# Optimization experiments

Hardware: AMD Instinct MI355X
Metric: run time of the kernel (lower is better)

Reference implementation:

```python
import jax, jax.numpy as jnp
import numpy as np
import math
from jax import lax

EPS = 1e-5  # BatchNorm1d default eps
K = 7       # causal conv kernel size
H = 5       # number of heads in block 2


def _cconv(x, w, b):
    # CausalConv1d: left-pad by (K-1)*dilation = 6, then valid conv. x: [B,C,L], w: [O,I,K]
    y = lax.conv_general_dilated(x, w, window_strides=(1,), padding=[(K - 1, 0)],
                                 dimension_numbers=('NCH', 'OIH', 'NCH'))
    return y + b[None, :, None]


def _bn(x, g, b):
    # BatchNorm1d in training mode: batch stats over (N, L) per channel, biased variance
    m = x.mean((0, 2), keepdims=True)
    v = ((x - m) ** 2).mean((0, 2), keepdims=True)
    return g[None, :, None] * (x - m) * lax.rsqrt(v + EPS) + b[None, :, None]


def _attn(x1, x2, x3, scale):
    # sigmoid(((X1 @ X2^T) / sqrt(L)) @ X3); x*: [B,C,L]
    s = jnp.einsum('bcl,bdl->bcd', x1, x2) * scale
    return jax.nn.sigmoid(jnp.einsum('bcd,bdl->bcl', s, x3))


def _attn_heads(x1, x2, x3, scale):
    # 5 heads chunked along L (contiguous chunks) -> vectorized over head axis
    B, C, L = x1.shape
    r = lambda x: x.reshape(B, C, H, L // H)
    x1r, x2r, x3r = r(x1), r(x2), r(x3)
    s = jnp.einsum('bchk,bdhk->bhcd', x1r, x2r) * scale  # scale uses full L, as in source
    a = jax.nn.sigmoid(jnp.einsum('bhcd,bdhk->bchk', s, x3r))
    return a.reshape(B, C, L)


def setup_inputs() -> dict:
    key = jax.random.key(0)
    ks = jax.random.split(key, 20)
    B, C, L = 64, 30, 200
    CL = C * L
    cs = (C * K) ** -0.5   # conv weight scale
    ls = CL ** -0.5        # linear weight scale
    d = {}
    d['X'] = jax.random.normal(ks[0], (B, C, L), jnp.float32)
    for i, nm in enumerate(['b1c1', 'b1c2', 'b1c3', 'b2c1', 'b2c2', 'b2c3']):
        d[nm + '_w'] = jax.random.normal(ks[1 + i], (C, C, K), jnp.float32) * cs
        d[nm + '_b'] = jax.random.normal(ks[7 + i], (C,), jnp.float32) * cs
    for nm in ['bn11', 'bn12', 'bn21', 'bn22']:
        d[nm + '_g'] = jnp.ones((C,), jnp.float32)
        d[nm + '_b'] = jnp.zeros((C,), jnp.float32)
    d['lin1_w'] = jax.random.normal(ks[13], (CL, CL), jnp.float32) * ls
    d['lin1_b'] = jax.random.normal(ks[14], (CL,), jnp.float32) * ls
    d['lin2_w'] = jax.random.normal(ks[15], (CL, CL), jnp.float32) * ls
    d['lin2_b'] = jax.random.normal(ks[16], (CL,), jnp.float32) * ls
    d['cw'] = jax.random.normal(ks[17], (CL, 2 * CL), jnp.float32) * (2 * CL) ** -0.5
    d['cb'] = jax.random.normal(ks[18], (CL,), jnp.float32) * (2 * CL) ** -0.5
    return d


def reference(X, b1c1_w, b1c1_b, b1c2_w, b1c2_b, b1c3_w, b1c3_b,
              bn11_g, bn11_b, lin1_w, lin1_b, lin2_w, lin2_b, bn12_g, bn12_b,
              b2c1_w, b2c1_b, b2c2_w, b2c2_b, b2c3_w, b2c3_b,
              bn21_g, bn21_b, bn22_g, bn22_b, cw, cb):
    B, C, L = X.shape
    scale = 1.0 / math.sqrt(L)
    # block 1: single-head sigmoid attention
    a1 = _attn(_cconv(X, b1c1_w, b1c1_b), _cconv(X, b1c2_w, b1c2_b),
               _cconv(X, b1c3_w, b1c3_b), scale)
    a1 = _bn(a1 + X, bn11_g, bn11_b)
    a1f = a1.reshape(B, -1)
    o1 = (a1f @ lin1_w.T + lin1_b) @ lin2_w.T + lin2_b  # dropout is eval-mode identity
    out1 = _bn(a1 + o1.reshape(B, C, L), bn12_g, bn12_b)
    # block 2: 5-head sigmoid attention
    a2 = _attn_heads(_cconv(X, b2c1_w, b2c1_b), _cconv(X, b2c2_w, b2c2_b),
                     _cconv(X, b2c3_w, b2c3_b), scale)
    a2 = _bn(a2 + X, bn21_g, bn21_b)
    a2f = a2.reshape(B, -1)
    # NOTE: source reuses b1_linearchain for block 2 (b2_linearchain is unused)
    o2 = (a2f @ lin1_w.T + lin1_b) @ lin2_w.T + lin2_b
    out2 = _bn(a2 + o2.reshape(B, C, L), bn22_g, bn22_b)
    # converge
    out = jnp.concatenate([out1, out2], axis=1).reshape(B, -1)  # [B, 2*C*L]
    out = out @ cw.T + cb                                       # [B, C*L]
    return out.reshape(B, 30, -1)
```

## Files before the change

### kernel.cpp

```cpp
#include <hip/hip_runtime.h>
#include <hip/hip_bf16.h>
#include <math.h>

typedef __attribute__((ext_vector_type(4))) float f32x4;
typedef __attribute__((ext_vector_type(8))) __bf16 bf16x8;
typedef __attribute__((ext_vector_type(8))) unsigned short u16x8;

__device__ __forceinline__ unsigned short f2bfu(float f) {
    unsigned u = __builtin_bit_cast(unsigned, f);
    u += 0x7fffu + ((u >> 16) & 1u);
    return (unsigned short)(u >> 16);
}

__device__ __forceinline__ bf16x8 to_bf8(f32x4 x, f32x4 y) {
    bf16x8 o;
#pragma unroll
    for (int j = 0; j < 4; ++j) { o[j] = (__bf16)x[j]; o[j + 4] = (__bf16)y[j]; }
    return o;
}

__device__ __forceinline__ void gload_lds16(const void* g, void* l) {
    __builtin_amdgcn_global_load_lds(
        (__attribute__((address_space(1))) const void*)g,
        (__attribute__((address_space(3))) void*)l, 16, 0, 0);
}

template <int VMPS>
__device__ __forceinline__ void wait_newer(int newer) {
    if (newer >= 2) {
        if constexpr (VMPS == 6) asm volatile("s_waitcnt vmcnt(12)" ::: "memory");
        else                     asm volatile("s_waitcnt vmcnt(10)" ::: "memory");
    } else if (newer == 1) {
        if constexpr (VMPS == 6) asm volatile("s_waitcnt vmcnt(6)" ::: "memory");
        else                     asm volatile("s_waitcnt vmcnt(5)" ::: "memory");
    } else {
        asm volatile("s_waitcnt vmcnt(0)" ::: "memory");
    }
}

struct ConvArgs {
    const float* w[6];
    const float* b[6];
};

__global__ __launch_bounds__(256) void conv_all(const float* __restrict__ X,
                                                ConvArgs args,
                                                float* __restrict__ out) {
    __shared__ float Xsp[30][208];
    __shared__ float Wg[30][212];
    const int b = blockIdx.x, j = blockIdx.y;
    const int tid = threadIdx.x;
    const float* xb = X + (size_t)b * 6000;
    for (int i = tid; i < 30 * 208; i += 256) {
        const int ci = i / 208, p = i - ci * 208;
        float v = 0.f;
        if (p >= 6 && p < 206) v = xb[ci * 200 + (p - 6)];
        Xsp[ci][p] = v;
    }
    const float* wsrc = args.w[j];
    for (int i = tid; i < 6300; i += 256) Wg[i / 210][i % 210] = wsrc[i];
    __syncthreads();
    if (tid < 240) {
        const int c = tid >> 3;
        const int strip = tid & 7;
        const int l0 = strip * 25;
        float acc[25];
        const float bias = args.b[j][c];
#pragma unroll
        for (int o = 0; o < 25; ++o) acc[o] = bias;
        for (int ci = 0; ci < 30; ++ci) {
            float wv[7];
#pragma unroll
            for (int kk = 0; kk < 7; ++kk) wv[kk] = Wg[c][ci * 7 + kk];
            float xw[31];
#pragma unroll
            for (int i = 0; i < 31; ++i) xw[i] = Xsp[ci][l0 + i];
#pragma unroll
            for (int o = 0; o < 25; ++o) {
                float a = acc[o];
#pragma unroll
                for (int kk = 0; kk < 7; ++kk) a += xw[o + kk] * wv[kk];
                acc[o] = a;
            }
        }
        float* op = out + ((size_t)j * 64 + b) * 6000 + c * 200 + l0;
#pragma unroll
        for (int o = 0; o < 25; ++o) op[o] = acc[o];
    }
}

__global__ __launch_bounds__(256) void attn_k(const float* __restrict__ conv,
                                              const float* __restrict__ X,
                                              float* __restrict__ A_lin) {
    __shared__ float x1s[30][204], x2s[30][204], x3s[30][204];
    __shared__ float S[5][30][30];
    const int b = blockIdx.x, blk = blockIdx.y;
    const int tid = threadIdx.x;
    const f32x4* c1 = (const f32x4*)(conv + (((size_t)blk * 3 + 0) * 64 + b) * 6000);
    const f32x4* c2 = (const f32x4*)(conv + (((size_t)blk * 3 + 1) * 64 + b) * 6000);
    const f32x4* c3 = (const f32x4*)(conv + (((size_t)blk * 3 + 2) * 64 + b) * 6000);
    for (int i = tid; i < 1500; i += 256) {
        const int c = i / 50, q = i - c * 50;
        *(f32x4*)&x1s[c][q * 4] = c1[i];
        *(f32x4*)&x2s[c][q * 4] = c2[i];
        *(f32x4*)&x3s[c][q * 4] = c3[i];
    }
    __syncthreads();
    const float scale = 7.0710678118654752e-2f;
    if (blk == 0) {
        for (int idx = tid; idx < 900; idx += 256) {
            const int c = idx / 30, d = idx - c * 30;
            f32x4 a4 = {};
            for (int q = 0; q < 50; ++q) {
                const f32x4 x = *(const f32x4*)&x1s[c][q * 4];
                const f32x4 y = *(const f32x4*)&x2s[d][q * 4];
                a4 += x * y;
            }
            S[0][c][d] = (a4[0] + a4[1] + a4[2] + a4[3]) * scale;
        }
    } else {
        for (int idx = tid; idx < 4500; idx += 256) {
            const int h = idx / 900, rem = idx - h * 900;
            const int c = rem / 30, d = rem - c * 30;
            f32x4 a4 = {};
            for (int q = 0; q < 10; ++q) {
                const f32x4 x = *(const f32x4*)&x1s[c][h * 40 + q * 4];
                const f32x4 y = *(const f32x4*)&x2s[d][h * 40 + q * 4];
                a4 += x * y;
            }
            S[h][c][d] = (a4[0] + a4[1] + a4[2] + a4[3]) * scale;
        }
    }
    __syncthreads();
    const float* Xb = X + (size_t)b * 6000;
    float* Ab = A_lin + ((size_t)blk * 64 + b) * 6000;
    for (int u = tid; u < 1500; u += 256) {
        const int c = u / 50, q = u - c * 50;
        const int hh = (blk == 0) ? 0 : (q / 10);
        f32x4 a4 = {};
        for (int d = 0; d < 30; ++d) {
            const float sv = S[hh][c][d];
            const f32x4 v = *(const f32x4*)&x3s[d][q * 4];
            a4 += sv * v;
        }
        const f32x4 xv = *(const f32x4*)(Xb + c * 200 + q * 4);
        f32x4 o;
#pragma unroll
        for (int jj = 0; jj < 4; ++jj)
            o[jj] = 1.f / (1.f + __expf(-a4[jj])) + xv[jj];
        *(f32x4*)(Ab + c * 200 + q * 4) = o;
    }
}

__global__ __launch_bounds__(256) void bn_fused1(float* __restrict__ A,
                                                 unsigned short* __restrict__ Ab,
                                                 const float* __restrict__ g11,
                                                 const float* __restrict__ b11,
                                                 const float* __restrict__ g21,
                                                 const float* __restrict__ b21) {
    const int c = blockIdx.x, h = blockIdx.y, bs = blockIdx.z;
    const int tid = threadIdx.x;
    const size_t cbase = (size_t)h * 64 * 6000 + c * 200;
    float s = 0.f, ss = 0.f;
    for (int i = tid; i < 12800; i += 256) {
        const int b = i / 200, l = i - b * 200;
        const float v = A[cbase + (size_t)b * 6000 + l];
        s += v; ss += v * v;
    }
    for (int off = 32; off > 0; off >>= 1) { s += __shfl_down(s, off); ss += __shfl_down(ss, off); }
    __shared__ float rs[4], rss[4];
    __shared__ float sc_sh, sh_sh;
    const int wave = tid >> 6, lane = tid & 63;
    if (lane == 0) { rs[wave] = s; rss[wave] = ss; }
    __syncthreads();
    if (tid == 0) {
        const float S = rs[0] + rs[1] + rs[2] + rs[3];
        const float SS = rss[0] + rss[1] + rss[2] + rss[3];
        const float mean = S * (1.f / 12800.f);
        const float var = SS * (1.f / 12800.f) - mean * mean;
        const float* gp = h ? g21 : g11;
        const float* bp = h ? b21 : b11;
        const float scale = gp[c] * rsqrtf(var + 1e-5f);
        sc_sh = scale;
        sh_sh = bp[c] - mean * scale;
    }
    __syncthreads();
    const float scale = sc_sh, shift = sh_sh;
    for (int i = tid; i < 1600; i += 256) {
        const int b = bs * 8 + i / 200, l = i % 200;
        const size_t idx = ((size_t)h * 64 + b) * 6000 + c * 200 + l;
        const float o = A[idx] * scale + shift;
        A[idx] = o;
        Ab[((size_t)h * 64 + b) * 6016 + c * 200 + l] = f2bfu(o);
    }
    if (c == 0) {
        for (int i = tid; i < 8 * 16; i += 256) {
            const int b = bs * 8 + (i >> 4);
            Ab[((size_t)h * 64 + b) * 6016 + 6000 + (i & 15)] = 0;
        }
    }
}

__global__ __launch_bounds__(256) void bn_fused2(const float* __restrict__ A,
                                                 const float* __restrict__ O,
                                                 unsigned short* __restrict__ Cat,
                                                 const float* __restrict__ g12,
                                                 const float* __restrict__ b12,
                                                 const float* __restrict__ g22,
                                                 const float* __restrict__ b22) {
    const int c = blockIdx.x, h = blockIdx.y, bs = blockIdx.z;
    const int tid = threadIdx.x;
    const size_t cbase = (size_t)h * 64 * 6000 + c * 200;
    float s = 0.f, ss = 0.f;
    for (int i = tid; i < 12800; i += 256) {
        const int b = i / 200, l = i - b * 200;
        const size_t idx = cbase + (size_t)b * 6000 + l;
        const float v = A[idx] + O[idx];
        s += v; ss += v * v;
    }
    for (int off = 32; off > 0; off >>= 1) { s += __shfl_down(s, off); ss += __shfl_down(ss, off); }
    __shared__ float rs[4], rss[4];
    __shared__ float sc_sh, sh_sh;
    const int wave = tid >> 6, lane = tid & 63;
    if (lane == 0) { rs[wave] = s; rss[wave] = ss; }
    __syncthreads();
    if (tid == 0) {
        const float S = rs[0] + rs[1] + rs[2] + rs[3];
        const float SS = rss[0] + rss[1] + rss[2] + rss[3];
        const float mean = S * (1.f / 12800.f);
        const float var = SS * (1.f / 12800.f) - mean * mean;
        const float* gp = h ? g22 : g12;
        const float* bp = h ? b22 : b12;
        const float scale = gp[c] * rsqrtf(var + 1e-5f);
        sc_sh = scale;
        sh_sh = bp[c] - mean * scale;
    }
    __syncthreads();
    const float scale = sc_sh, shift = sh_sh;
    for (int i = tid; i < 1600; i += 256) {
        const int b = bs * 8 + i / 200, l = i % 200;
        const size_t idx = ((size_t)h * 64 + b) * 6000 + c * 200 + l;
        const float o = (A[idx] + O[idx]) * scale + shift;
        Cat[(size_t)b * 12000 + (size_t)h * 6000 + c * 200 + l] = f2bfu(o);
    }
}

template <int MT>
__global__ __launch_bounds__(256) void gemm_pipe(const unsigned short* __restrict__ A,
                                                 const float* __restrict__ W,
                                                 unsigned short* __restrict__ P,
                                                 int N, int K, int KA,
                                                 int iters_total, int iters_per) {
    constexpr int M = MT * 16;
    constexpr int WB = 128 * 32 * 4;
    constexpr int AB = M * 32 * 2;
    constexpr int ACH = AB / 1024;
    constexpr int BUFSZ = WB + AB;
    constexpr int VMPS = 4 + ACH / 4;
    __shared__ __align__(16) char lds[3][BUFSZ];

    const int tid = threadIdx.x;
    const int wave = tid >> 6;
    const int lane = tid & 63;
    const int r = lane & 15;
    const int g = lane >> 4;
    const int n0 = blockIdx.x * 128;
    const int s = blockIdx.y;
    const int it0 = s * iters_per;
    int it1 = it0 + iters_per;
    if (it1 > iters_total) it1 = iters_total;
    const int nst = it1 - it0;

    f32x4 acc[MT][2] = {};

    const float* wbase[4];
    const float* wclamp[4];
    int kth[4];
#pragma unroll
    for (int u = 0; u < 4; ++u) {
        const int c = wave + 4 * u;
        const int slot = c * 64 + lane;
        const int row = slot >> 3, jj = slot & 7;
        const int j = jj ^ (row & 7);
        int rn = n0 + row;
        if (rn > N - 1) rn = N - 1;
        wbase[u] = W + (size_t)rn * K + j * 4;
        wclamp[u] = W + (size_t)rn * K + (K - 4);
        kth[u] = K - 4 - j * 4;
    }
    const unsigned short* abase[ACH / 4];
#pragma unroll
    for (int u = 0; u < ACH / 4; ++u) {
        const int c = wave + 4 * u;
        const int slot = c * 64 + lane;
        const int m = slot >> 2, jj = slot & 3;
        const int j = jj ^ ((m >> 1) & 3);
        abase[u] = A + (size_t)m * KA + j * 8;
    }

    auto stage = [&](char* base, int it) {
        const int k0 = it * 32;
#pragma unroll
        for (int u = 0; u < 4; ++u) {
            const float* src = (k0 <= kth[u]) ? (wbase[u] + k0) : wclamp[u];
            gload_lds16(src, base + (wave + 4 * u) * 1024);
        }
        char* ab = base + WB;
#pragma unroll
        for (int u = 0; u < ACH / 4; ++u) {
            gload_lds16(abase[u] + k0, ab + (wave + 4 * u) * 1024);
        }
    };

    auto compute = [&](const char* base) {
        const float* Wb = (const float*)base;
        const unsigned short* Ab = (const unsigned short*)(base + WB);
        bf16x8 bfrag[2];
#pragma unroll
        for (int nt = 0; nt < 2; ++nt) {
            const int wr = (wave + 4 * nt) * 16 + r;
            const f32x4* Wrow = (const f32x4*)(Wb + wr * 32);
            bfrag[nt] = to_bf8(Wrow[(2 * g) ^ (r & 7)], Wrow[(2 * g + 1) ^ (r & 7)]);
        }
#pragma unroll
        for (int mt = 0; mt < MT; ++mt) {
            const int m = mt * 16 + r;
            const bf16x8 afrag = __builtin_bit_cast(
                bf16x8, ((const u16x8*)(Ab + (size_t)m * 32))[g ^ ((m >> 1) & 3)]);
            acc[mt][0] = __builtin_amdgcn_mfma_f32_16x16x32_bf16(afrag, bfrag[0], acc[mt][0], 0, 0, 0);
            acc[mt][1] = __builtin_amdgcn_mfma_f32_16x16x32_bf16(afrag, bfrag[1], acc[mt][1], 0, 0, 0);
        }
    };

    if (nst > 0) {
        const int p = nst < 3 ? nst : 3;
        stage(&lds[0][0], it0);
        if (p > 1) stage(&lds[1][0], it0 + 1);
        if (p > 2) stage(&lds[2][0], it0 + 2);
        wait_newer<VMPS>(p - 1);
        __builtin_amdgcn_s_barrier();
        __builtin_amdgcn_sched_barrier(0);

        int bi = 0;
        for (int it = it0; it < it1; ++it) {
            compute(&lds[bi][0]);
            __builtin_amdgcn_sched_barrier(0);
            __builtin_amdgcn_s_barrier();
            if (it + 3 < it1) stage(&lds[bi][0], it + 3);
            if (it + 1 < it1) {
                const int last = it1 - 1;
                const int newer = ((it + 3 < last ? it + 3 : last)) - (it + 1);
                wait_newer<VMPS>(newer);
                __builtin_amdgcn_s_barrier();
                __builtin_amdgcn_sched_barrier(0);
            }
            bi = bi == 2 ? 0 : bi + 1;
        }
    }

    unsigned short* Pp = P + (size_t)s * M * N;
#pragma unroll
    for (int nt = 0; nt < 2; ++nt) {
        const int col = n0 + (wave + 4 * nt) * 16 + r;
        if (col < N) {
#pragma unroll
            for (int mt = 0; mt < MT; ++mt) {
#pragma unroll
                for (int rr = 0; rr < 4; ++rr) {
                    const int row = mt * 16 + g * 4 + rr;
                    Pp[(size_t)row * N + col] = f2bfu(acc[mt][nt][rr]);
                }
            }
        }
    }
}

template <bool OUT_BF16>
__global__ __launch_bounds__(256) void reduce_bias(const unsigned short* __restrict__ P,
                                                   const float* __restrict__ bias,
                                                   int KS, int MN, int N, int KOUT,
                                                   float* __restrict__ of,
                                                   unsigned short* __restrict__ ob) {
    const int gid0 = blockIdx.x * 256 + threadIdx.x;
    const int gstr = gridDim.x * 256;
    for (int idx = gid0; idx < MN; idx += gstr) {
        float v = bias[idx % N];
        for (int s = 0; s < KS; ++s) {
            const unsigned u = P[(size_t)s * MN + idx];
            v += __builtin_bit_cast(float, u << 16);
        }
        if constexpr (OUT_BF16) ob[(size_t)(idx / N) * KOUT + (idx % N)] = f2bfu(v);
        else of[idx] = v;
    }
    if constexpr (OUT_BF16) {
        if (KOUT > N) {
            const int M = MN / N, PADW = KOUT - N;
            for (int i = gid0; i < M * PADW; i += gstr)
                ob[(size_t)(i / PADW) * KOUT + N + (i % PADW)] = 0;
        }
    }
}

extern "C" void kernel_launch(void* const* d_in, const int* in_sizes, int n_in,
                              void* d_out, int out_size, void* d_ws, size_t ws_size,
                              hipStream_t stream) {
    (void)in_sizes; (void)n_in; (void)out_size;
    const float* X = (const float*)d_in[0];
    ConvArgs ca;
    for (int j = 0; j < 6; ++j) {
        ca.w[j] = (const float*)d_in[1 + 2 * j];
        ca.b[j] = (const float*)d_in[2 + 2 * j];
    }
    const float* bn11_g = (const float*)d_in[13];
    const float* bn11_b = (const float*)d_in[14];
    const float* bn12_g = (const float*)d_in[15];
    const float* bn12_b = (const float*)d_in[16];
    const float* bn21_g = (const float*)d_in[17];
    const float* bn21_b = (const float*)d_in[18];
    const float* bn22_g = (const float*)d_in[19];
    const float* bn22_b = (const float*)d_in[20];
    const float* lin1_w = (const float*)d_in[21];
    const float* lin1_b = (const float*)d_in[22];
    const float* lin2_w = (const float*)d_in[23];
    const float* lin2_b = (const float*)d_in[24];
    const float* cw = (const float*)d_in[25];
    const float* cb = (const float*)d_in[26];
    float* out = (float*)d_out;

    char* w = (char*)d_ws;
    float* A_lin = (float*)w;
    unsigned short* A_bf = (unsigned short*)(w + 3072000);
    char* U = w + 4612096;
    float* convout = (float*)U;
    unsigned short* T_bf = (unsigned short*)U;
    float* O = (float*)(U + 1540096);
    unsigned short* Cat = (unsigned short*)(U + 4612096);
    unsigned short* P = (unsigned short*)(w + 13832192);

    const size_t avail = ws_size > 13832192 ? ws_size - 13832192 : 0;
    int KS12 = (int)(avail / 1536000);
    if (KS12 > 10) KS12 = 10;
    if (KS12 < 1) KS12 = 1;
    int KS3 = (int)(avail / 768000);
    if (KS3 > 10) KS3 = 10;
    if (KS3 < 1) KS3 = 1;

    conv_all<<<dim3(64, 6), 256, 0, stream>>>(X, ca, convout);
    attn_k<<<dim3(64, 2), 256, 0, stream>>>(convout, X, A_lin);
    bn_fused1<<<dim3(30, 2, 8), 256, 0, stream>>>(A_lin, A_bf, bn11_g, bn11_b, bn21_g, bn21_b);

    {
        const int it_tot = 188;
        const int it_per = (it_tot + KS12 - 1) / KS12;
        gemm_pipe<8><<<dim3(47, KS12), 256, 0, stream>>>(A_bf, lin1_w, P, 6000, 6000, 6016, it_tot, it_per);
        reduce_bias<true><<<dim3(768), 256, 0, stream>>>(P, lin1_b, KS12, 768000, 6000, 6016, nullptr, T_bf);
        gemm_pipe<8><<<dim3(47, KS12), 256, 0, stream>>>(T_bf, lin2_w, P, 6000, 6000, 6016, it_tot, it_per);
        reduce_bias<false><<<dim3(768), 256, 0, stream>>>(P, lin2_b, KS12, 768000, 6000, 6000, O, nullptr);
    }

    bn_fused2<<<dim3(30, 2, 8), 256, 0, stream>>>(A_lin, O, Cat, bn12_g, bn12_b, bn22_g, bn22_b);

    {
        const int it_tot = 375;
        const int it_per = (it_tot + KS3 - 1) / KS3;
        gemm_pipe<4><<<dim3(47, KS3), 256, 0, stream>>>(Cat, cw, P, 6000, 12000, 12000, it_tot, it_per);
        reduce_bias<false><<<dim3(768), 256, 0, stream>>>(P, cb, KS3, 384000, 6000, 6000, out, nullptr);
    }
}
```

Before: 257.9 us.

## Retile weight-streaming GEMM to 64-wide N, 64-deep K with double buffering

Changes the GEMM tile from 128 output columns by 32 K to 64 columns by 64 K, with a new XOR swizzle and a two-stage instead of three-stage LDS pipeline. It doubles the number of N-blocks, lowers the split-K factors, and pads the concatenated activation rows to 12032 with zeroed tails so the final GEMM's K loop stays aligned. The aim is more blocks across CUs, fewer partial sums to reduce and fewer barriers per byte of weights streamed. The cost is less prefetch depth and less reuse of A per W tile.

```diff
diff --git a/kernel.cpp b/kernel.cpp
--- a/kernel.cpp
+++ b/kernel.cpp
@@ -25,17 +25,11 @@
         (__attribute__((address_space(3))) void*)l, 16, 0, 0);
 }
 
-template <int VMPS>
-__device__ __forceinline__ void wait_newer(int newer) {
-    if (newer >= 2) {
-        if constexpr (VMPS == 6) asm volatile("s_waitcnt vmcnt(12)" ::: "memory");
-        else                     asm volatile("s_waitcnt vmcnt(10)" ::: "memory");
-    } else if (newer == 1) {
-        if constexpr (VMPS == 6) asm volatile("s_waitcnt vmcnt(6)" ::: "memory");
-        else                     asm volatile("s_waitcnt vmcnt(5)" ::: "memory");
-    } else {
-        asm volatile("s_waitcnt vmcnt(0)" ::: "memory");
-    }
+template <int N>
+__device__ __forceinline__ void waitcnt_vm() {
+    if constexpr (N == 8)      asm volatile("s_waitcnt vmcnt(8)" ::: "memory");
+    else if constexpr (N == 6) asm volatile("s_waitcnt vmcnt(6)" ::: "memory");
+    else                       asm volatile("s_waitcnt vmcnt(0)" ::: "memory");
 }
 
 struct ConvArgs {
@@ -241,7 +235,13 @@
         const int b = bs * 8 + i / 200, l = i % 200;
         const size_t idx = ((size_t)h * 64 + b) * 6000 + c * 200 + l;
         const float o = (A[idx] + O[idx]) * scale + shift;
-        Cat[(size_t)b * 12000 + (size_t)h * 6000 + c * 200 + l] = f2bfu(o);
+        Cat[(size_t)b * 12032 + (size_t)h * 6000 + c * 200 + l] = f2bfu(o);
+    }
+    if (c == 0 && h == 0) {
+        for (int i = tid; i < 8 * 32; i += 256) {
+            const int b = bs * 8 + (i >> 5);
+            Cat[(size_t)b * 12032 + 12000 + (i & 31)] = 0;
+        }
     }
 }
 
@@ -252,26 +252,26 @@
                                                  int N, int K, int KA,
                                                  int iters_total, int iters_per) {
     constexpr int M = MT * 16;
-    constexpr int WB = 128 * 32 * 4;
-    constexpr int AB = M * 32 * 2;
-    constexpr int ACH = AB / 1024;
+    constexpr int WB = 64 * 64 * 4;
+    constexpr int AB = M * 64 * 2;
+    constexpr int ACH_PW = (AB / 1024) / 4;
     constexpr int BUFSZ = WB + AB;
-    constexpr int VMPS = 4 + ACH / 4;
-    __shared__ __align__(16) char lds[3][BUFSZ];
+    constexpr int VMPS = 4 + ACH_PW;
+    __shared__ __align__(16) char lds[2][BUFSZ];
 
     const int tid = threadIdx.x;
     const int wave = tid >> 6;
     const int lane = tid & 63;
     const int r = lane & 15;
     const int g = lane >> 4;
-    const int n0 = blockIdx.x * 128;
+    const int n0 = blockIdx.x * 64;
     const int s = blockIdx.y;
     const int it0 = s * iters_per;
     int it1 = it0 + iters_per;
     if (it1 > iters_total) it1 = iters_total;
     const int nst = it1 - it0;
 
-    f32x4 acc[MT][2] = {};
+    f32x4 acc[MT] = {};
 
     const float* wbase[4];
     const float* wclamp[4];
@@ -279,27 +279,27 @@
 #pragma unroll
     for (int u = 0; u < 4; ++u) {
         const int c = wave + 4 * u;
-        const int slot = c * 64 + lane;
-        const int row = slot >> 3, jj = slot & 7;
-        const int j = jj ^ (row & 7);
+        const int row = c * 4 + (lane >> 4);
+        const int jj = lane & 15;
+        const int j = jj ^ (row & 15);
         int rn = n0 + row;
         if (rn > N - 1) rn = N - 1;
         wbase[u] = W + (size_t)rn * K + j * 4;
         wclamp[u] = W + (size_t)rn * K + (K - 4);
         kth[u] = K - 4 - j * 4;
     }
-    const unsigned short* abase[ACH / 4];
-#pragma unroll
-    for (int u = 0; u < ACH / 4; ++u) {
+    const unsigned short* abase[ACH_PW];
+#pragma unroll
+    for (int u = 0; u < ACH_PW; ++u) {
         const int c = wave + 4 * u;
-        const int slot = c * 64 + lane;
-        const int m = slot >> 2, jj = slot & 3;
-        const int j = jj ^ ((m >> 1) & 3);
+        const int m = c * 8 + (lane >> 3);
+        const int jj = lane & 7;
+        const int j = jj ^ (m & 7);
         abase[u] = A + (size_t)m * KA + j * 8;
     }
 
     auto stage = [&](char* base, int it) {
-        const int k0 = it * 32;
+        const int k0 = it * 64;
 #pragma unroll
         for (int u = 0; u < 4; ++u) {
             const float* src = (k0 <= kth[u]) ? (wbase[u] + k0) : wclamp[u];
@@ -307,7 +307,7 @@
         }
         char* ab = base + WB;
 #pragma unroll
-        for (int u = 0; u < ACH / 4; ++u) {
+        for (int u = 0; u < ACH_PW; ++u) {
             gload_lds16(abase[u] + k0, ab + (wave + 4 * u) * 1024);
         }
     };
@@ -315,61 +315,59 @@
     auto compute = [&](const char* base) {
         const float* Wb = (const float*)base;
         const unsigned short* Ab = (const unsigned short*)(base + WB);
-        bf16x8 bfrag[2];
-#pragma unroll
-        for (int nt = 0; nt < 2; ++nt) {
-            const int wr = (wave + 4 * nt) * 16 + r;
-            const f32x4* Wrow = (const f32x4*)(Wb + wr * 32);
-            bfrag[nt] = to_bf8(Wrow[(2 * g) ^ (r & 7)], Wrow[(2 * g + 1) ^ (r & 7)]);
-        }
-#pragma unroll
-        for (int mt = 0; mt < MT; ++mt) {
-            const int m = mt * 16 + r;
-            const bf16x8 afrag = __builtin_bit_cast(
-                bf16x8, ((const u16x8*)(Ab + (size_t)m * 32))[g ^ ((m >> 1) & 3)]);
-            acc[mt][0] = __builtin_amdgcn_mfma_f32_16x16x32_bf16(afrag, bfrag[0], acc[mt][0], 0, 0, 0);
-            acc[mt][1] = __builtin_amdgcn_mfma_f32_16x16x32_bf16(afrag, bfrag[1], acc[mt][1], 0, 0, 0);
+        const float* Wrow = Wb + (wave * 16 + r) * 64;
+        const unsigned short* Arow0 = Ab + (size_t)r * 64;
+#pragma unroll
+        for (int ks = 0; ks < 2; ++ks) {
+            const f32x4 x = ((const f32x4*)Wrow)[(2 * g + 8 * ks) ^ r];
+            const f32x4 y = ((const f32x4*)Wrow)[(2 * g + 1 + 8 * ks) ^ r];
+            const bf16x8 bfrag = to_bf8(x, y);
+            const int ai = (ks * 4 + g) ^ (r & 7);
+#pragma unroll
+            for (int mt = 0; mt < MT; ++mt) {
+                const bf16x8 afrag = __builtin_bit_cast(
+                    bf16x8, ((const u16x8*)(Arow0 + (size_t)mt * 1024))[ai]);
+                acc[mt] = __builtin_amdgcn_mfma_f32_16x16x32_bf16(afrag, bfrag, acc[mt], 0, 0, 0);
+            }
         }
     };
 
     if (nst > 0) {
-        const int p = nst < 3 ? nst : 3;
         stage(&lds[0][0], it0);
-        if (p > 1) stage(&lds[1][0], it0 + 1);
-        if (p > 2) stage(&lds[2][0], it0 + 2);
-        wait_newer<VMPS>(p - 1);
+        if (nst > 1) {
+            stage(&lds[1][0], it0 + 1);
+            waitcnt_vm<VMPS>();
+        } else {
+            waitcnt_vm<0>();
+        }
         __builtin_amdgcn_s_barrier();
         __builtin_amdgcn_sched_barrier(0);
 
-        int bi = 0;
+        int cur = 0;
         for (int it = it0; it < it1; ++it) {
-            compute(&lds[bi][0]);
+            compute(&lds[cur][0]);
             __builtin_amdgcn_sched_barrier(0);
             __builtin_amdgcn_s_barrier();
-            if (it + 3 < it1) stage(&lds[bi][0], it + 3);
+            if (it + 2 < it1) stage(&lds[cur][0], it + 2);
             if (it + 1 < it1) {
-                const int last = it1 - 1;
-                const int newer = ((it + 3 < last ? it + 3 : last)) - (it + 1);
-                wait_newer<VMPS>(newer);
+                if (it + 2 < it1) waitcnt_vm<VMPS>();
+                else              waitcnt_vm<0>();
                 __builtin_amdgcn_s_barrier();
                 __builtin_amdgcn_sched_barrier(0);
             }
-            bi = bi == 2 ? 0 : bi + 1;
+            cur ^= 1;
         }
     }
 
     unsigned short* Pp = P + (size_t)s * M * N;
-#pragma unroll
-    for (int nt = 0; nt < 2; ++nt) {
-        const int col = n0 + (wave + 4 * nt) * 16 + r;
-        if (col < N) {
-#pragma unroll
-            for (int mt = 0; mt < MT; ++mt) {
-#pragma unroll
-                for (int rr = 0; rr < 4; ++rr) {
-                    const int row = mt * 16 + g * 4 + rr;
-                    Pp[(size_t)row * N + col] = f2bfu(acc[mt][nt][rr]);
-                }
+    const int col = n0 + wave * 16 + r;
+    if (col < N) {
+#pragma unroll
+        for (int mt = 0; mt < MT; ++mt) {
+#pragma unroll
+            for (int rr = 0; rr < 4; ++rr) {
+                const int row = mt * 16 + g * 4 + rr;
+                Pp[(size_t)row * N + col] = f2bfu(acc[mt][rr]);
             }
         }
     }
@@ -439,10 +437,10 @@
 
     const size_t avail = ws_size > 13832192 ? ws_size - 13832192 : 0;
     int KS12 = (int)(avail / 1536000);
-    if (KS12 > 10) KS12 = 10;
+    if (KS12 > 5) KS12 = 5;
     if (KS12 < 1) KS12 = 1;
     int KS3 = (int)(avail / 768000);
-    if (KS3 > 10) KS3 = 10;
+    if (KS3 > 8) KS3 = 8;
     if (KS3 < 1) KS3 = 1;
 
     conv_all<<<dim3(64, 6), 256, 0, stream>>>(X, ca, convout);
@@ -450,20 +448,20 @@
     bn_fused1<<<dim3(30, 2, 8), 256, 0, stream>>>(A_lin, A_bf, bn11_g, bn11_b, bn21_g, bn21_b);
 
     {
+        const int it_tot = 94;
+        const int it_per = (it_tot + KS12 - 1) / KS12;
+        gemm_pipe<8><<<dim3(94, KS12), 256, 0, stream>>>(A_bf, lin1_w, P, 6000, 6000, 6016, it_tot, it_per);
+        reduce_bias<true><<<dim3(768), 256, 0, stream>>>(P, lin1_b, KS12, 768000, 6000, 6016, nullptr, T_bf);
+        gemm_pipe<8><<<dim3(94, KS12), 256, 0, stream>>>(T_bf, lin2_w, P, 6000, 6000, 6016, it_tot, it_per);
+        reduce_bias<false><<<dim3(768), 256, 0, stream>>>(P, lin2_b, KS12, 768000, 6000, 6000, O, nullptr);
+    }
+
+    bn_fused2<<<dim3(30, 2, 8), 256, 0, stream>>>(A_lin, O, Cat, bn12_g, bn12_b, bn22_g, bn22_b);
+
+    {
         const int it_tot = 188;
-        const int it_per = (it_tot + KS12 - 1) / KS12;
-        gemm_pipe<8><<<dim3(47, KS12), 256, 0, stream>>>(A_bf, lin1_w, P, 6000, 6000, 6016, it_tot, it_per);
-        reduce_bias<true><<<dim3(768), 256, 0, stream>>>(P, lin1_b, KS12, 768000, 6000, 6016, nullptr, T_bf);
-        gemm_pipe<8><<<dim3(47, KS12), 256, 0, stream>>>(T_bf, lin2_w, P, 6000, 6000, 6016, it_tot, it_per);
-        reduce_bias<false><<<dim3(768), 256, 0, stream>>>(P, lin2_b, KS12, 768000, 6000, 6000, O, nullptr);
-    }
-
-    bn_fused2<<<dim3(30, 2, 8), 256, 0, stream>>>(A_lin, O, Cat, bn12_g, bn12_b, bn22_g, bn22_b);
-
-    {
-        const int it_tot = 375;
         const int it_per = (it_tot + KS3 - 1) / KS3;
-        gemm_pipe<4><<<dim3(47, KS3), 256, 0, stream>>>(Cat, cw, P, 6000, 12000, 12000, it_tot, it_per);
+        gemm_pipe<4><<<dim3(94, KS3), 256, 0, stream>>>(Cat, cw, P, 6000, 12000, 12032, it_tot, it_per);
         reduce_bias<false><<<dim3(768), 256, 0, stream>>>(P, cb, KS3, 384000, 6000, 6000, out, nullptr);
     }
 }
```

Result: faster. 240.2 us, median of 2 (-6.9%).
